# Optimization experiments

Measured on AMD Instinct MI355X. Metric: run time of the kernel, lower is better.

Reference implementation:

```python
import jax, jax.numpy as jnp
import numpy as np

STRIDE = 2
PAD = 1
K = 4
OUT_PAD = 0


def setup_inputs() -> dict:
    key = jax.random.key(0)
    k1, k2, k3, k4 = jax.random.split(key, 4)
    x = jax.random.normal(k1, (16, 64, 128, 128), dtype=jnp.float32)
    # torch ConvTranspose2d weight layout: [in_channels, out_channels, kH, kW]
    w = jax.random.normal(k2, (64, 32, 4, 4), dtype=jnp.float32) * 0.05
    conv_b = jax.random.normal(k3, (32,), dtype=jnp.float32) * 0.05
    bias = jax.random.normal(k4, (1, 1, 1, 1), dtype=jnp.float32)
    return {"x": x, "w": w, "conv_b": conv_b, "bias": bias}


def conv_transpose2d(x, w, conv_b):
    # Equivalent of torch ConvTranspose2d(k=4, s=2, p=1, op=0):
    # dilate input by stride, pad by k-1-p (+op on trailing side), conv with flipped kernel.
    lo = K - 1 - PAD
    hi = K - 1 - PAD + OUT_PAD
    w_oihw = jnp.flip(w, axis=(2, 3)).transpose(1, 0, 2, 3)  # [Cout, Cin, kH, kW]
    y = jax.lax.conv_general_dilated(
        x, w_oihw,
        window_strides=(1, 1),
        padding=((lo, hi), (lo, hi)),
        lhs_dilation=(STRIDE, STRIDE),
        dimension_numbers=("NCHW", "OIHW", "NCHW"),
    )
    return y + conv_b[None, :, None, None]


def reference(x, w, conv_b, bias):
    y = conv_transpose2d(x, w, conv_b)          # [N, Cout, H', W']
    y = jnp.min(y, axis=1, keepdims=True)       # channel-min -> [N,1,H',W']
    y = jnp.sum(y, axis=2, keepdims=True)       # height-sum  -> [N,1,1,W']
    # kernel uses tanh-based GELU approximation
    return jax.nn.gelu(y, approximate=True) + bias
```

## Files before the change

kernel.cpp:

```cpp
#include <hip/hip_runtime.h>
#include <math.h>

typedef __attribute__((ext_vector_type(8))) short short8;
typedef __attribute__((ext_vector_type(16))) float f32x16;
typedef __attribute__((ext_vector_type(2))) unsigned uintx2;

#define XS_STRIDE 72
#define NROWS 10

__device__ __forceinline__ short f2bf(float f) {
    union { float f; unsigned u; } v; v.f = f;
    unsigned r = (v.u + 0x7FFFu + ((v.u >> 16) & 1u)) >> 16;
    return (short)r;
}

__device__ __forceinline__ unsigned cvt_pk_bf16(float lo, float hi) {
    unsigned r;
    asm("v_cvt_pk_bf16_f32 %0, %1, %2" : "=v"(r) : "v"(lo), "v"(hi));
    return r;
}

__device__ __forceinline__ void bar_lds() {
    asm volatile("s_waitcnt lgkmcnt(0)" ::: "memory");
    __builtin_amdgcn_s_barrier();
}

__global__ void prep(const float* __restrict__ w, short* __restrict__ wfrag) {
    int idx = blockIdx.x * 256 + threadIdx.x;
    int j    = idx & 7;
    int lane = (idx >> 3) & 63;
    int q    = (idx >> 9) & 15;
    int p    = idx >> 13;
    int co = lane & 31, hf = lane >> 5;
    int ci = (q & 3) * 16 + hf * 8 + j;
    int tq = q >> 2, a = tq >> 1, b = tq & 1;
    int ph = p >> 1, pw = p & 1;
    int kh = 2 * a + 1 - ph, kw = 2 * b + 1 - pw;
    wfrag[idx] = f2bf(w[((ci * 32 + co) * 4 + kh) * 4 + kw]);
}

__global__ __launch_bounds__(256, 3) void convt_mfma(
    const float* __restrict__ x, const short* __restrict__ wfrag,
    const float* __restrict__ conv_b, float* __restrict__ partials)
{
    __shared__ short xs[NROWS][34][XS_STRIDE];
    __shared__ float minbuf[4][32];

    int blk = ((blockIdx.x & 7) << 7) | (blockIdx.x >> 3);
    const int jq = blk & 3;
    const int st = (blk >> 2) & 15;
    const int n  = blk >> 6;
    const int t  = threadIdx.x;
    const int i0 = st * 8;

    const int wv = t >> 6, lane = t & 63;
    const int ph = wv >> 1, pw = wv & 1;
    const int ln = lane & 31, half = lane >> 5;

    short8 af[16];
    {
        const short8* wf = (const short8*)(wfrag + wv * 8192);
        #pragma unroll
        for (int q = 0; q < 16; ++q) af[q] = wf[q * 64 + lane];
    }
    float cb[16];
    #pragma unroll
    for (int reg = 0; reg < 16; ++reg)
        cb[reg] = conv_b[(reg & 3) + 8 * (reg >> 2) + 4 * half];

    const float* xn = x + (size_t)n * 64 * 128 * 128;

    const int col  = t & 31;
    const int cib  = (t >> 5) * 8;
    const int gcol = jq * 32 + col;

    float hv[5];
    #pragma unroll
    for (int q = 0; q < 5; ++q) {
        int idx = q * 256 + t;
        int r = idx >> 7, side = (idx >> 6) & 1, ci = idx & 63;
        int gi = i0 - 1 + r;
        int gc = jq * 32 + (side ? 32 : -1);
        hv[q] = ((unsigned)gi < 128u && (unsigned)gc < 128u)
              ? xn[((size_t)ci * 128 + gi) * 128 + gc] : 0.f;
    }

    float pfA[8], pfB[8];
    auto load_row = [&](int r, float* dst) {
        int gi = i0 - 1 + r;
        bool rowok = (unsigned)gi < 128u;
        int gic = rowok ? gi : 0;
        const float* px = xn + ((size_t)cib * 128 + gic) * 128 + gcol;
        #pragma unroll
        for (int c = 0; c < 8; ++c) dst[c] = rowok ? px[c * 16384] : 0.f;
    };
    auto write_row = [&](int r, const float* src) {
        uintx2 u0, u1;
        u0.x = cvt_pk_bf16(src[0], src[1]); u0.y = cvt_pk_bf16(src[2], src[3]);
        u1.x = cvt_pk_bf16(src[4], src[5]); u1.y = cvt_pk_bf16(src[6], src[7]);
        *(uintx2*)&xs[r][col + 1][cib]     = u0;
        *(uintx2*)&xs[r][col + 1][cib + 4] = u1;
    };
    load_row(0, pfA);
    load_row(1, pfB);
    #pragma unroll
    for (int r = 0; r < NROWS; r += 2) {
        write_row(r, pfA);
        if (r + 2 < NROWS) load_row(r + 2, pfA);
        write_row(r + 1, pfB);
        if (r + 3 < NROWS) load_row(r + 3, pfB);
    }
    #pragma unroll
    for (int q = 0; q < 5; ++q) {
        int idx = q * 256 + t;
        int r = idx >> 7, side = (idx >> 6) & 1, ci = idx & 63;
        xs[r][side ? 33 : 0][ci] = f2bf(hv[q]);
    }

    bar_lds();

    float osum = 0.f;
    #pragma unroll
    for (int k = 0; k < 4; ++k) {
        const int L0 = 2 * k + ph;
        f32x16 acc0, acc1;
        #pragma unroll
        for (int reg = 0; reg < 16; ++reg) { acc0[reg] = cb[reg]; acc1[reg] = cb[reg]; }
        __builtin_amdgcn_s_setprio(1);
        #pragma unroll
        for (int b = 0; b < 2; ++b) {
            int colp = ln + (pw - b) + 1;
            const short* p0 = &xs[L0][colp][half * 8];
            const short* p1 = &xs[L0 + 1][colp][half * 8];
            const short* p2 = &xs[L0 + 2][colp][half * 8];
            #pragma unroll
            for (int c = 0; c < 4; ++c) {
                short8 Fs = *(const short8*)(p1 + c * 16);
                acc0 = __builtin_amdgcn_mfma_f32_32x32x16_bf16(af[4*b+c],   Fs, acc0, 0, 0, 0);
                acc1 = __builtin_amdgcn_mfma_f32_32x32x16_bf16(af[8+4*b+c], Fs, acc1, 0, 0, 0);
                short8 F0 = *(const short8*)(p0 + c * 16);
                acc0 = __builtin_amdgcn_mfma_f32_32x32x16_bf16(af[8+4*b+c], F0, acc0, 0, 0, 0);
                short8 F2 = *(const short8*)(p2 + c * 16);
                acc1 = __builtin_amdgcn_mfma_f32_32x32x16_bf16(af[4*b+c],   F2, acc1, 0, 0, 0);
            }
        }
        __builtin_amdgcn_s_setprio(0);

        float mn0, mn1;
        {
            float a = fminf(fminf(acc0[0], acc0[1]), fminf(acc0[2], acc0[3]));
            float b2 = fminf(fminf(acc0[4], acc0[5]), fminf(acc0[6], acc0[7]));
            float c = fminf(fminf(acc0[8], acc0[9]), fminf(acc0[10], acc0[11]));
            float d = fminf(fminf(acc0[12], acc0[13]), fminf(acc0[14], acc0[15]));
            mn0 = fminf(fminf(a, b2), fminf(c, d));
            a = fminf(fminf(acc1[0], acc1[1]), fminf(acc1[2], acc1[3]));
            b2 = fminf(fminf(acc1[4], acc1[5]), fminf(acc1[6], acc1[7]));
            c = fminf(fminf(acc1[8], acc1[9]), fminf(acc1[10], acc1[11]));
            d = fminf(fminf(acc1[12], acc1[13]), fminf(acc1[14], acc1[15]));
            mn1 = fminf(fminf(a, b2), fminf(c, d));
        }
        mn0 = fminf(mn0, __shfl_xor(mn0, 32, 64));
        mn1 = fminf(mn1, __shfl_xor(mn1, 32, 64));
        osum += mn0 + mn1;
    }

    if (half == 0) minbuf[wv][ln] = osum;
    bar_lds();

    if (t < 64) {
        int c = t & 31, pwp = t >> 5;
        float v = minbuf[pwp][c] + minbuf[2 + pwp][c];
        int ow = ((jq * 32 + c) << 1) | pwp;
        partials[(size_t)st * 4096 + n * 256 + ow] = v;
    }
}

__global__ void finalize(const float* __restrict__ partials,
                         const float* __restrict__ bias, float* __restrict__ out)
{
    int idx = blockIdx.x * 256 + threadIdx.x;
    float s = 0.f;
    #pragma unroll
    for (int st = 0; st < 16; ++st) s += partials[st * 4096 + idx];
    float u = 0.7978845608028654f * (s + 0.044715f * s * s * s);
    out[idx] = 0.5f * s * (1.f + tanhf(u)) + bias[0];
}

extern "C" void kernel_launch(void* const* d_in, const int* in_sizes, int n_in,
                              void* d_out, int out_size, void* d_ws, size_t ws_size,
                              hipStream_t stream) {
    const float* x      = (const float*)d_in[0];
    const float* w      = (const float*)d_in[1];
    const float* conv_b = (const float*)d_in[2];
    const float* bias   = (const float*)d_in[3];
    float* out = (float*)d_out;

    short* wfrag    = (short*)d_ws;
    float* partials = (float*)((char*)d_ws + 65536);

    hipLaunchKernelGGL(prep, dim3(128), dim3(256), 0, stream, w, wfrag);
    hipLaunchKernelGGL(convt_mfma, dim3(16 * 16 * 4), dim3(256), 0, stream,
                       x, wfrag, conv_b, partials);
    hipLaunchKernelGGL(finalize, dim3(16), dim3(256), 0, stream,
                       partials, bias, out);
}
```

Measured before the change: 115.8 us.

## Pre-transpose input to padded bf16 NHWC and stage via direct global-to-LDS loads

A new pre-pass kernel converts x to bf16 in a zero-padded, channel-innermost layout with an XOR swizzle, and computes the weight fragments in the same launch. The MFMA kernel then fills LDS with global_load_lds DMA copies instead of strided fp32 gathers plus in-register conversion, and reads LDS through the matching swizzle. This adds a full extra write and read of a bf16 copy of x (about half the size of the fp32 input) through a workspace buffer, trading extra HBM traffic for simpler, coalesced staging in the main kernel.

Result: slower. 125.6 us (+8.5%).

```diff
diff --git a/kernel.cpp b/kernel.cpp
--- a/kernel.cpp
+++ b/kernel.cpp
@@ -3,10 +3,11 @@
 
 typedef __attribute__((ext_vector_type(8))) short short8;
 typedef __attribute__((ext_vector_type(16))) float f32x16;
-typedef __attribute__((ext_vector_type(2))) unsigned uintx2;
-
-#define XS_STRIDE 72
-#define NROWS 10
+typedef __attribute__((ext_vector_type(4))) unsigned uintx4;
+
+#define XT_ROWSH 8320
+#define XT_NSH   (130 * 8320)
+#define XS_ROWB  4352
 
 __device__ __forceinline__ short f2bf(float f) {
     union { float f; unsigned u; } v; v.f = f;
@@ -25,31 +26,75 @@
     __builtin_amdgcn_s_barrier();
 }
 
-__global__ void prep(const float* __restrict__ w, short* __restrict__ wfrag) {
-    int idx = blockIdx.x * 256 + threadIdx.x;
-    int j    = idx & 7;
-    int lane = (idx >> 3) & 63;
-    int q    = (idx >> 9) & 15;
-    int p    = idx >> 13;
-    int co = lane & 31, hf = lane >> 5;
-    int ci = (q & 3) * 16 + hf * 8 + j;
-    int tq = q >> 2, a = tq >> 1, b = tq & 1;
-    int ph = p >> 1, pw = p & 1;
-    int kh = 2 * a + 1 - ph, kw = 2 * b + 1 - pw;
-    wfrag[idx] = f2bf(w[((ci * 32 + co) * 4 + kh) * 4 + kw]);
+__device__ __forceinline__ void gload_lds16(const void* g, void* l) {
+    __builtin_amdgcn_global_load_lds(
+        (const __attribute__((address_space(1))) unsigned*)g,
+        (__attribute__((address_space(3))) unsigned*)l, 16, 0, 0);
+}
+__device__ __forceinline__ void gload_lds4(const void* g, void* l) {
+    __builtin_amdgcn_global_load_lds(
+        (const __attribute__((address_space(1))) unsigned*)g,
+        (__attribute__((address_space(3))) unsigned*)l, 4, 0, 0);
+}
+
+__global__ void cvt_t(const float* __restrict__ x, const float* __restrict__ w,
+                      short* __restrict__ wfrag, short* __restrict__ xt)
+{
+    int blk = blockIdx.x;
+    int t = threadIdx.x;
+    if (blk >= 16 * 130) {
+        int idx = (blk - 16 * 130) * 256 + t;
+        int j    = idx & 7;
+        int lane = (idx >> 3) & 63;
+        int q    = (idx >> 9) & 15;
+        int p    = idx >> 13;
+        int co = lane & 31, hf = lane >> 5;
+        int ci = (q & 3) * 16 + hf * 8 + j;
+        int tq = q >> 2, a = tq >> 1, b = tq & 1;
+        int ph = p >> 1, pw = p & 1;
+        int kh = 2 * a + 1 - ph, kw = 2 * b + 1 - pw;
+        wfrag[idx] = f2bf(w[((ci * 32 + co) * 4 + kh) * 4 + kw]);
+        return;
+    }
+    int n = blk / 130, prow = blk - n * 130;
+    short* xr = xt + (size_t)n * XT_NSH + (size_t)prow * XT_ROWSH;
+
+    if (prow == 0 || prow == 129) {
+        for (int i = t; i < 1040; i += 256)
+            *(uintx4*)(xr + i * 8) = (uintx4)0;
+        return;
+    }
+    if (t < 16) {
+        int side = t >> 3, o = t & 7;
+        *(uintx4*)(xr + (side ? 129 * 64 : 0) + o * 8) = (uintx4)0;
+    }
+    int row = prow - 1;
+    const float* xb = x + (size_t)n * 64 * 128 * 128 + row * 128;
+    int col = t & 31, ci8 = (t >> 5) * 8;
+    #pragma unroll
+    for (int qd = 0; qd < 4; ++qd) {
+        int c0 = col + 32 * qd, pcol = c0 + 1;
+        const float* px = xb + (size_t)ci8 * 16384 + c0;
+        float v[8];
+        #pragma unroll
+        for (int c = 0; c < 8; ++c) v[c] = px[(size_t)c * 16384];
+        uintx4 u;
+        u.x = cvt_pk_bf16(v[0], v[1]); u.y = cvt_pk_bf16(v[2], v[3]);
+        u.z = cvt_pk_bf16(v[4], v[5]); u.w = cvt_pk_bf16(v[6], v[7]);
+        int off = (ci8 * 2) ^ ((pcol & 7) << 4);
+        *(uintx4*)((char*)xr + (size_t)pcol * 128 + off) = u;
+    }
 }
 
 __global__ __launch_bounds__(256, 3) void convt_mfma(
-    const float* __restrict__ x, const short* __restrict__ wfrag,
+    const short* __restrict__ xt, const short* __restrict__ wfrag,
     const float* __restrict__ conv_b, float* __restrict__ partials)
 {
-    __shared__ short xs[NROWS][34][XS_STRIDE];
+    __shared__ short xs[10 * 34 * 64];
     __shared__ float minbuf[4][32];
 
     int blk = ((blockIdx.x & 7) << 7) | (blockIdx.x >> 3);
-    const int jq = blk & 3;
-    const int st = (blk >> 2) & 15;
-    const int n  = blk >> 6;
+    const int jq = blk & 3, st = (blk >> 2) & 15, n = blk >> 6;
     const int t  = threadIdx.x;
     const int i0 = st * 8;
 
@@ -68,56 +113,19 @@
     for (int reg = 0; reg < 16; ++reg)
         cb[reg] = conv_b[(reg & 3) + 8 * (reg >> 2) + 4 * half];
 
-    const float* xn = x + (size_t)n * 64 * 128 * 128;
-
-    const int col  = t & 31;
-    const int cib  = (t >> 5) * 8;
-    const int gcol = jq * 32 + col;
-
-    float hv[5];
-    #pragma unroll
-    for (int q = 0; q < 5; ++q) {
-        int idx = q * 256 + t;
-        int r = idx >> 7, side = (idx >> 6) & 1, ci = idx & 63;
-        int gi = i0 - 1 + r;
-        int gc = jq * 32 + (side ? 32 : -1);
-        hv[q] = ((unsigned)gi < 128u && (unsigned)gc < 128u)
-              ? xn[((size_t)ci * 128 + gi) * 128 + gc] : 0.f;
-    }
-
-    float pfA[8], pfB[8];
-    auto load_row = [&](int r, float* dst) {
-        int gi = i0 - 1 + r;
-        bool rowok = (unsigned)gi < 128u;
-        int gic = rowok ? gi : 0;
-        const float* px = xn + ((size_t)cib * 128 + gic) * 128 + gcol;
-        #pragma unroll
-        for (int c = 0; c < 8; ++c) dst[c] = rowok ? px[c * 16384] : 0.f;
-    };
-    auto write_row = [&](int r, const float* src) {
-        uintx2 u0, u1;
-        u0.x = cvt_pk_bf16(src[0], src[1]); u0.y = cvt_pk_bf16(src[2], src[3]);
-        u1.x = cvt_pk_bf16(src[4], src[5]); u1.y = cvt_pk_bf16(src[6], src[7]);
-        *(uintx2*)&xs[r][col + 1][cib]     = u0;
-        *(uintx2*)&xs[r][col + 1][cib + 4] = u1;
-    };
-    load_row(0, pfA);
-    load_row(1, pfB);
-    #pragma unroll
-    for (int r = 0; r < NROWS; r += 2) {
-        write_row(r, pfA);
-        if (r + 2 < NROWS) load_row(r + 2, pfA);
-        write_row(r + 1, pfB);
-        if (r + 3 < NROWS) load_row(r + 3, pfB);
-    }
-    #pragma unroll
-    for (int q = 0; q < 5; ++q) {
-        int idx = q * 256 + t;
-        int r = idx >> 7, side = (idx >> 6) & 1, ci = idx & 63;
-        xs[r][side ? 33 : 0][ci] = f2bf(hv[q]);
-    }
-
-    bar_lds();
+    {
+        const char* xtn = (const char*)(xt + (size_t)n * XT_NSH);
+        for (int r = wv; r < 10; r += 4) {
+            const char* src = xtn + (size_t)(i0 + r) * (XT_ROWSH * 2)
+                            + (size_t)(jq * 32) * 128;
+            char* dst = (char*)xs + r * XS_ROWB;
+            #pragma unroll
+            for (int ch = 0; ch < 4; ++ch)
+                gload_lds16(src + ch * 1024 + lane * 16, dst + ch * 1024);
+            gload_lds4(src + 4096 + lane * 4, dst + 4096);
+        }
+    }
+    __syncthreads();
 
     float osum = 0.f;
     #pragma unroll
@@ -130,17 +138,19 @@
         #pragma unroll
         for (int b = 0; b < 2; ++b) {
             int colp = ln + (pw - b) + 1;
-            const short* p0 = &xs[L0][colp][half * 8];
-            const short* p1 = &xs[L0 + 1][colp][half * 8];
-            const short* p2 = &xs[L0 + 2][colp][half * 8];
+            unsigned swz = (unsigned)(colp & 7) << 4;
+            const char* r0 = (const char*)xs + (L0    ) * XS_ROWB + colp * 128;
+            const char* r1 = (const char*)xs + (L0 + 1) * XS_ROWB + colp * 128;
+            const char* r2 = (const char*)xs + (L0 + 2) * XS_ROWB + colp * 128;
             #pragma unroll
             for (int c = 0; c < 4; ++c) {
-                short8 Fs = *(const short8*)(p1 + c * 16);
+                unsigned offp = ((unsigned)(half * 16 + c * 32)) ^ swz;
+                short8 Fs = *(const short8*)(r1 + offp);
                 acc0 = __builtin_amdgcn_mfma_f32_32x32x16_bf16(af[4*b+c],   Fs, acc0, 0, 0, 0);
                 acc1 = __builtin_amdgcn_mfma_f32_32x32x16_bf16(af[8+4*b+c], Fs, acc1, 0, 0, 0);
-                short8 F0 = *(const short8*)(p0 + c * 16);
+                short8 F0 = *(const short8*)(r0 + offp);
                 acc0 = __builtin_amdgcn_mfma_f32_32x32x16_bf16(af[8+4*b+c], F0, acc0, 0, 0, 0);
-                short8 F2 = *(const short8*)(p2 + c * 16);
+                short8 F2 = *(const short8*)(r2 + offp);
                 acc1 = __builtin_amdgcn_mfma_f32_32x32x16_bf16(af[4*b+c],   F2, acc1, 0, 0, 0);
             }
         }
@@ -197,10 +207,12 @@
 
     short* wfrag    = (short*)d_ws;
     float* partials = (float*)((char*)d_ws + 65536);
-
-    hipLaunchKernelGGL(prep, dim3(128), dim3(256), 0, stream, w, wfrag);
+    short* xt       = (short*)((char*)d_ws + 65536 + 262144);
+
+    hipLaunchKernelGGL(cvt_t, dim3(16 * 130 + 128), dim3(256), 0, stream,
+                       x, w, wfrag, xt);
     hipLaunchKernelGGL(convt_mfma, dim3(16 * 16 * 4), dim3(256), 0, stream,
-                       x, wfrag, conv_b, partials);
+                       xt, wfrag, conv_b, partials);
     hipLaunchKernelGGL(finalize, dim3(16), dim3(256), 0, stream,
                        partials, bias, out);
 }
```

## Fuse finalize into conv kernel via last-block counter; deepen row prefetch

Applied to the files above, without the earlier changes.

Removes the separate finalize launch. Each block bumps a per-batch atomic counter after writing its partials, and the last of the 64 blocks for a batch sums the 16 strips and applies GELU plus bias. The counters are zeroed by an extra block in the prep kernel. The x row prefetch goes from two to four register buffers, and the halo and weight-fragment loads move after the main row loads so more global loads are in flight. This trades one kernel launch for atomics, fences and more register pressure, which could lower occupancy.

Measured after the change: 202.4 us. +74.9%, slower.

```diff
diff --git a/kernel.cpp b/kernel.cpp
--- a/kernel.cpp
+++ b/kernel.cpp
@@ -25,7 +25,12 @@
     __builtin_amdgcn_s_barrier();
 }
 
-__global__ void prep(const float* __restrict__ w, short* __restrict__ wfrag) {
+__global__ void prep(const float* __restrict__ w, short* __restrict__ wfrag,
+                     unsigned* __restrict__ ctr) {
+    if (blockIdx.x >= 128) {
+        if (threadIdx.x < 16) ctr[threadIdx.x] = 0u;
+        return;
+    }
     int idx = blockIdx.x * 256 + threadIdx.x;
     int j    = idx & 7;
     int lane = (idx >> 3) & 63;
@@ -41,15 +46,16 @@
 
 __global__ __launch_bounds__(256, 3) void convt_mfma(
     const float* __restrict__ x, const short* __restrict__ wfrag,
-    const float* __restrict__ conv_b, float* __restrict__ partials)
+    const float* __restrict__ conv_b, float* __restrict__ partials,
+    unsigned* __restrict__ ctr, const float* __restrict__ bias,
+    float* __restrict__ out)
 {
     __shared__ short xs[NROWS][34][XS_STRIDE];
     __shared__ float minbuf[4][32];
+    __shared__ unsigned lastf;
 
     int blk = ((blockIdx.x & 7) << 7) | (blockIdx.x >> 3);
-    const int jq = blk & 3;
-    const int st = (blk >> 2) & 15;
-    const int n  = blk >> 6;
+    const int jq = blk & 3, st = (blk >> 2) & 15, n = blk >> 6;
     const int t  = threadIdx.x;
     const int i0 = st * 8;
 
@@ -57,35 +63,12 @@
     const int ph = wv >> 1, pw = wv & 1;
     const int ln = lane & 31, half = lane >> 5;
 
-    short8 af[16];
-    {
-        const short8* wf = (const short8*)(wfrag + wv * 8192);
-        #pragma unroll
-        for (int q = 0; q < 16; ++q) af[q] = wf[q * 64 + lane];
-    }
-    float cb[16];
-    #pragma unroll
-    for (int reg = 0; reg < 16; ++reg)
-        cb[reg] = conv_b[(reg & 3) + 8 * (reg >> 2) + 4 * half];
-
     const float* xn = x + (size_t)n * 64 * 128 * 128;
-
     const int col  = t & 31;
     const int cib  = (t >> 5) * 8;
     const int gcol = jq * 32 + col;
 
-    float hv[5];
-    #pragma unroll
-    for (int q = 0; q < 5; ++q) {
-        int idx = q * 256 + t;
-        int r = idx >> 7, side = (idx >> 6) & 1, ci = idx & 63;
-        int gi = i0 - 1 + r;
-        int gc = jq * 32 + (side ? 32 : -1);
-        hv[q] = ((unsigned)gi < 128u && (unsigned)gc < 128u)
-              ? xn[((size_t)ci * 128 + gi) * 128 + gc] : 0.f;
-    }
-
-    float pfA[8], pfB[8];
+    float pf0[8], pf1[8], pf2[8], pf3[8];
     auto load_row = [&](int r, float* dst) {
         int gi = i0 - 1 + r;
         bool rowok = (unsigned)gi < 128u;
@@ -101,14 +84,27 @@
         *(uintx2*)&xs[r][col + 1][cib]     = u0;
         *(uintx2*)&xs[r][col + 1][cib + 4] = u1;
     };
-    load_row(0, pfA);
-    load_row(1, pfB);
-    #pragma unroll
-    for (int r = 0; r < NROWS; r += 2) {
-        write_row(r, pfA);
-        if (r + 2 < NROWS) load_row(r + 2, pfA);
-        write_row(r + 1, pfB);
-        if (r + 3 < NROWS) load_row(r + 3, pfB);
+    load_row(0, pf0); load_row(1, pf1); load_row(2, pf2); load_row(3, pf3);
+    write_row(0, pf0); load_row(4, pf0);
+    write_row(1, pf1); load_row(5, pf1);
+    write_row(2, pf2); load_row(6, pf2);
+    write_row(3, pf3); load_row(7, pf3);
+    write_row(4, pf0); load_row(8, pf0);
+    write_row(5, pf1); load_row(9, pf1);
+    write_row(6, pf2);
+    write_row(7, pf3);
+    write_row(8, pf0);
+    write_row(9, pf1);
+
+    float hv[5];
+    #pragma unroll
+    for (int q = 0; q < 5; ++q) {
+        int idx = q * 256 + t;
+        int r = idx >> 7, side = (idx >> 6) & 1, ci = idx & 63;
+        int gi = i0 - 1 + r;
+        int gc = jq * 32 + (side ? 32 : -1);
+        hv[q] = ((unsigned)gi < 128u && (unsigned)gc < 128u)
+              ? xn[((size_t)ci * 128 + gi) * 128 + gc] : 0.f;
     }
     #pragma unroll
     for (int q = 0; q < 5; ++q) {
@@ -116,6 +112,17 @@
         int r = idx >> 7, side = (idx >> 6) & 1, ci = idx & 63;
         xs[r][side ? 33 : 0][ci] = f2bf(hv[q]);
     }
+
+    short8 af[16];
+    {
+        const short8* wf = (const short8*)(wfrag + wv * 8192);
+        #pragma unroll
+        for (int q = 0; q < 16; ++q) af[q] = wf[q * 64 + lane];
+    }
+    float cb[16];
+    #pragma unroll
+    for (int reg = 0; reg < 16; ++reg)
+        cb[reg] = conv_b[(reg & 3) + 8 * (reg >> 2) + 4 * half];
 
     bar_lds();
 
@@ -171,19 +178,25 @@
         int c = t & 31, pwp = t >> 5;
         float v = minbuf[pwp][c] + minbuf[2 + pwp][c];
         int ow = ((jq * 32 + c) << 1) | pwp;
-        partials[(size_t)st * 4096 + n * 256 + ow] = v;
-    }
-}
-
-__global__ void finalize(const float* __restrict__ partials,
-                         const float* __restrict__ bias, float* __restrict__ out)
-{
-    int idx = blockIdx.x * 256 + threadIdx.x;
-    float s = 0.f;
-    #pragma unroll
-    for (int st = 0; st < 16; ++st) s += partials[st * 4096 + idx];
-    float u = 0.7978845608028654f * (s + 0.044715f * s * s * s);
-    out[idx] = 0.5f * s * (1.f + tanhf(u)) + bias[0];
+        __hip_atomic_store(&partials[(size_t)st * 4096 + n * 256 + ow], v,
+                           __ATOMIC_RELAXED, __HIP_MEMORY_SCOPE_AGENT);
+    }
+    __threadfence();
+    __syncthreads();
+    if (t == 0) lastf = (atomicAdd(&ctr[n], 1u) == 63u) ? 1u : 0u;
+    __syncthreads();
+
+    if (lastf) {
+        __threadfence();
+        float b0 = bias[0];
+        float s = 0.f;
+        #pragma unroll
+        for (int s2 = 0; s2 < 16; ++s2)
+            s += __hip_atomic_load(&partials[(size_t)s2 * 4096 + n * 256 + t],
+                                   __ATOMIC_RELAXED, __HIP_MEMORY_SCOPE_AGENT);
+        float u = 0.7978845608028654f * (s + 0.044715f * s * s * s);
+        out[n * 256 + t] = 0.5f * s * (1.f + tanhf(u)) + b0;
+    }
 }
 
 extern "C" void kernel_launch(void* const* d_in, const int* in_sizes, int n_in,
@@ -195,12 +208,11 @@
     const float* bias   = (const float*)d_in[3];
     float* out = (float*)d_out;
 
-    short* wfrag    = (short*)d_ws;
-    float* partials = (float*)((char*)d_ws + 65536);
-
-    hipLaunchKernelGGL(prep, dim3(128), dim3(256), 0, stream, w, wfrag);
+    short*    wfrag    = (short*)d_ws;
+    float*    partials = (float*)((char*)d_ws + 65536);
+    unsigned* ctr      = (unsigned*)((char*)d_ws + 65536 + 262144);
+
+    hipLaunchKernelGGL(prep, dim3(129), dim3(256), 0, stream, w, wfrag, ctr);
     hipLaunchKernelGGL(convt_mfma, dim3(16 * 16 * 4), dim3(256), 0, stream,
-                       x, wfrag, conv_b, partials);
-    hipLaunchKernelGGL(finalize, dim3(16), dim3(256), 0, stream,
-                       partials, bias, out);
-}
+                       x, wfrag, conv_b, partials, ctr, bias, out);
+}
```

## Fuse finalize into conv kernel via atomic accumulation and last-block epilogue

Applied to the files above, without the earlier changes.

Removes the separate finalize launch. Each block now atomically adds its height-partial sums into a per-batch accumulator, and a per-batch counter picks the last finishing block to apply GELU and bias. Accumulator and counter zeroing is folded into the prep kernel as an extra block. The global loads are also reordered so the main row loads are issued before the halo loads and the weight-fragment loads. The float atomics make the summation order nondeterministic and add atomic traffic and an extra block barrier.

After: 113.7 us. About the same (-1.8%).

```diff
diff --git a/kernel.cpp b/kernel.cpp
--- a/kernel.cpp
+++ b/kernel.cpp
@@ -25,7 +25,14 @@
     __builtin_amdgcn_s_barrier();
 }
 
-__global__ void prep(const float* __restrict__ w, short* __restrict__ wfrag) {
+__global__ void prep(const float* __restrict__ w, short* __restrict__ wfrag,
+                     float* __restrict__ acc, unsigned* __restrict__ ctr) {
+    if (blockIdx.x >= 128) {
+        #pragma unroll
+        for (int i = 0; i < 16; ++i) acc[i * 256 + threadIdx.x] = 0.f;
+        if (threadIdx.x < 16) ctr[threadIdx.x] = 0u;
+        return;
+    }
     int idx = blockIdx.x * 256 + threadIdx.x;
     int j    = idx & 7;
     int lane = (idx >> 3) & 63;
@@ -41,15 +48,16 @@
 
 __global__ __launch_bounds__(256, 3) void convt_mfma(
     const float* __restrict__ x, const short* __restrict__ wfrag,
-    const float* __restrict__ conv_b, float* __restrict__ partials)
+    const float* __restrict__ conv_b, float* __restrict__ acc,
+    unsigned* __restrict__ ctr, const float* __restrict__ bias,
+    float* __restrict__ out)
 {
     __shared__ short xs[NROWS][34][XS_STRIDE];
     __shared__ float minbuf[4][32];
+    __shared__ unsigned lastf;
 
     int blk = ((blockIdx.x & 7) << 7) | (blockIdx.x >> 3);
-    const int jq = blk & 3;
-    const int st = (blk >> 2) & 15;
-    const int n  = blk >> 6;
+    const int jq = blk & 3, st = (blk >> 2) & 15, n = blk >> 6;
     const int t  = threadIdx.x;
     const int i0 = st * 8;
 
@@ -57,33 +65,10 @@
     const int ph = wv >> 1, pw = wv & 1;
     const int ln = lane & 31, half = lane >> 5;
 
-    short8 af[16];
-    {
-        const short8* wf = (const short8*)(wfrag + wv * 8192);
-        #pragma unroll
-        for (int q = 0; q < 16; ++q) af[q] = wf[q * 64 + lane];
-    }
-    float cb[16];
-    #pragma unroll
-    for (int reg = 0; reg < 16; ++reg)
-        cb[reg] = conv_b[(reg & 3) + 8 * (reg >> 2) + 4 * half];
-
     const float* xn = x + (size_t)n * 64 * 128 * 128;
-
     const int col  = t & 31;
     const int cib  = (t >> 5) * 8;
     const int gcol = jq * 32 + col;
-
-    float hv[5];
-    #pragma unroll
-    for (int q = 0; q < 5; ++q) {
-        int idx = q * 256 + t;
-        int r = idx >> 7, side = (idx >> 6) & 1, ci = idx & 63;
-        int gi = i0 - 1 + r;
-        int gc = jq * 32 + (side ? 32 : -1);
-        hv[q] = ((unsigned)gi < 128u && (unsigned)gc < 128u)
-              ? xn[((size_t)ci * 128 + gi) * 128 + gc] : 0.f;
-    }
 
     float pfA[8], pfB[8];
     auto load_row = [&](int r, float* dst) {
@@ -110,12 +95,34 @@
         write_row(r + 1, pfB);
         if (r + 3 < NROWS) load_row(r + 3, pfB);
     }
+
+    float hv[5];
+    #pragma unroll
+    for (int q = 0; q < 5; ++q) {
+        int idx = q * 256 + t;
+        int r = idx >> 7, side = (idx >> 6) & 1, ci = idx & 63;
+        int gi = i0 - 1 + r;
+        int gc = jq * 32 + (side ? 32 : -1);
+        hv[q] = ((unsigned)gi < 128u && (unsigned)gc < 128u)
+              ? xn[((size_t)ci * 128 + gi) * 128 + gc] : 0.f;
+    }
     #pragma unroll
     for (int q = 0; q < 5; ++q) {
         int idx = q * 256 + t;
         int r = idx >> 7, side = (idx >> 6) & 1, ci = idx & 63;
         xs[r][side ? 33 : 0][ci] = f2bf(hv[q]);
     }
+
+    short8 af[16];
+    {
+        const short8* wf = (const short8*)(wfrag + wv * 8192);
+        #pragma unroll
+        for (int q = 0; q < 16; ++q) af[q] = wf[q * 64 + lane];
+    }
+    float cb[16];
+    #pragma unroll
+    for (int reg = 0; reg < 16; ++reg)
+        cb[reg] = conv_b[(reg & 3) + 8 * (reg >> 2) + 4 * half];
 
     bar_lds();
 
@@ -171,19 +178,19 @@
         int c = t & 31, pwp = t >> 5;
         float v = minbuf[pwp][c] + minbuf[2 + pwp][c];
         int ow = ((jq * 32 + c) << 1) | pwp;
-        partials[(size_t)st * 4096 + n * 256 + ow] = v;
-    }
-}
-
-__global__ void finalize(const float* __restrict__ partials,
-                         const float* __restrict__ bias, float* __restrict__ out)
-{
-    int idx = blockIdx.x * 256 + threadIdx.x;
-    float s = 0.f;
-    #pragma unroll
-    for (int st = 0; st < 16; ++st) s += partials[st * 4096 + idx];
-    float u = 0.7978845608028654f * (s + 0.044715f * s * s * s);
-    out[idx] = 0.5f * s * (1.f + tanhf(u)) + bias[0];
+        atomicAdd(&acc[n * 256 + ow], v);
+    }
+    __syncthreads();
+    if (t == 0) lastf = (atomicAdd(&ctr[n], 1u) == 63u) ? 1u : 0u;
+    __syncthreads();
+
+    if (lastf) {
+        __threadfence();
+        float s = __hip_atomic_load(&acc[n * 256 + t], __ATOMIC_RELAXED,
+                                    __HIP_MEMORY_SCOPE_AGENT);
+        float u = 0.7978845608028654f * (s + 0.044715f * s * s * s);
+        out[n * 256 + t] = 0.5f * s * (1.f + tanhf(u)) + bias[0];
+    }
 }
 
 extern "C" void kernel_launch(void* const* d_in, const int* in_sizes, int n_in,
@@ -195,12 +202,11 @@
     const float* bias   = (const float*)d_in[3];
     float* out = (float*)d_out;
 
-    short* wfrag    = (short*)d_ws;
-    float* partials = (float*)((char*)d_ws + 65536);
-
-    hipLaunchKernelGGL(prep, dim3(128), dim3(256), 0, stream, w, wfrag);
+    short*    wfrag = (short*)d_ws;
+    float*    acc   = (float*)((char*)d_ws + 65536);
+    unsigned* ctr   = (unsigned*)((char*)d_ws + 65536 + 16384);
+
+    hipLaunchKernelGGL(prep, dim3(129), dim3(256), 0, stream, w, wfrag, acc, ctr);
     hipLaunchKernelGGL(convt_mfma, dim3(16 * 16 * 4), dim3(256), 0, stream,
-                       x, wfrag, conv_b, partials);
-    hipLaunchKernelGGL(finalize, dim3(16), dim3(256), 0, stream,
-                       partials, bias, out);
-}
+                       x, wfrag, conv_b, acc, ctr, bias, out);
+}
```
